# Kernel tuning notes

Hardware: AMD Instinct MI355X
Metric: run time of the kernel (lower is better)

The kernel has to match this reference:

```python
import jax, jax.numpy as jnp
import numpy as np

BN_EPS = 1e-5


def setup_inputs() -> dict:
    key = jax.random.key(0)
    ks = jax.random.split(key, 8)
    N, H, OUT = 32 * 1024, 512, 32
    return {
        "x": jax.random.normal(ks[0], (N, 2), dtype=jnp.float32),
        "batch_size": 32,
        "Wq": jax.random.normal(ks[1], (2, H), dtype=jnp.float32) / np.sqrt(2.0),
        "Wk": jax.random.normal(ks[2], (2, H), dtype=jnp.float32) / np.sqrt(2.0),
        "Wv": jax.random.normal(ks[3], (2, H), dtype=jnp.float32) / np.sqrt(2.0),
        "bn_gamma": jnp.ones((H,), jnp.float32),
        "bn_beta": jnp.zeros((H,), jnp.float32),
        "bn_mean": jnp.zeros((H,), jnp.float32),
        "bn_var": jnp.ones((H,), jnp.float32),
        "prelu_a": jnp.full((1,), 0.25, jnp.float32),
        "W_out": jax.random.normal(ks[4], (H, OUT), dtype=jnp.float32) / np.sqrt(H),
        "b_out": jnp.zeros((OUT,), jnp.float32),
    }


def reference(x, batch_size, Wq, Wk, Wv, bn_gamma, bn_beta, bn_mean, bn_var,
              prelu_a, W_out, b_out):
    H = Wq.shape[1]
    # project tokens [N,2] -> [B,S,H]
    q = (x @ Wq).reshape(batch_size, -1, H)
    k = (x @ Wk).reshape(batch_size, -1, H)
    v = (x @ Wv).reshape(batch_size, -1, H)
    scale = 1.0 / jnp.sqrt(jnp.asarray(H, x.dtype))
    attn = jax.nn.softmax(jnp.einsum("bqh,bkh->bqk", q, k) * scale, axis=-1)
    out = jnp.einsum("bqk,bkh->bqh", attn, v).reshape(-1, H)  # [N,H]
    # BatchNorm1d (eval mode) + PReLU + Linear (dropout = identity in eval)
    out = (out - bn_mean) * (bn_gamma / jnp.sqrt(bn_var + BN_EPS)) + bn_beta
    out = jnp.where(out >= 0, out, prelu_a[0] * out)
    return out @ W_out + b_out
```

## Files before the change

### kernel.cpp

```cpp
#include <hip/hip_runtime.h>
#include <math.h>


#define H_DIM   512
#define OUT_DIM 32
#define S_LEN   1024
#define THREADS 256
#define NW 4

#if __has_builtin(__builtin_amdgcn_exp2f)
#define EXP2(x) __builtin_amdgcn_exp2f(x)
#else
#define EXP2(x) exp2f(x)
#endif

typedef __attribute__((ext_vector_type(8))) short bf16x8;
typedef __attribute__((ext_vector_type(4))) float f32x4;
typedef __attribute__((ext_vector_type(2))) float f32x2;

__device__ __forceinline__ f32x2 pkfma(f32x2 a, f32x2 b, f32x2 c) {
    return __builtin_elementwise_fma(a, b, c);
}
__device__ __forceinline__ unsigned int cvt_pk_bf16(float lo, float hi) {
    unsigned int r;
    asm("v_cvt_pk_bf16_f32 %0, %1, %2" : "=v"(r) : "v"(lo), "v"(hi));
    return r;
}

union frag_cast { unsigned int u[4]; int4 i4; bf16x8 v; };

__global__ __launch_bounds__(THREADS)
void fused_attn_kernel(const float* __restrict__ x,
                       const float* __restrict__ Wq,
                       const float* __restrict__ Wk,
                       const float* __restrict__ Wv,
                       const float* __restrict__ bn_gamma,
                       const float* __restrict__ bn_beta,
                       const float* __restrict__ bn_mean,
                       const float* __restrict__ bn_var,
                       const float* __restrict__ prelu_a,
                       const float* __restrict__ Wout,
                       const float* __restrict__ bout,
                       float* __restrict__ out)
{
    __shared__ __align__(16) float xsx[S_LEN];
    __shared__ __align__(16) float xsy[S_LEN];
    __shared__ float4 a01s[H_DIM / 2];
    __shared__ float2 cps[H_DIM / 2];
    __shared__ unsigned int bfr[32 * 64 * 4];
    __shared__ float redl[NW][64], redw0[NW][64], redw1[NW][64];
    __shared__ float mred[NW][4];

    const int t    = threadIdx.x;
    const int lane = t & 63;
    const int q    = __builtin_amdgcn_readfirstlane(t >> 6);
    const int b    = blockIdx.x >> 4;
    const int tile = blockIdx.x & 15;
    const float scale = 0.044194173824159216f;
    const float L2E   = 1.4426950408889634f;

    const float4* xg = (const float4*)(x + (size_t)b * (S_LEN * 2));
    f32x2* xsx2 = (f32x2*)xsx;
    f32x2* xsy2 = (f32x2*)xsy;
    {
        float4 v0 = xg[t];
        float4 v1 = xg[t + 256];
        f32x2 a = {v0.x, v0.z}; xsx2[t] = a;
        f32x2 c = {v0.y, v0.w}; xsy2[t] = c;
        f32x2 d = {v1.x, v1.z}; xsx2[t + 256] = d;
        f32x2 e = {v1.y, v1.w}; xsy2[t + 256] = e;
    }

    {
        const float2 gm = ((const float2*)bn_gamma)[t];
        const float2 vr = ((const float2*)bn_var)[t];
        const float2 bt = ((const float2*)bn_beta)[t];
        const float2 mn = ((const float2*)bn_mean)[t];
        const float2 wv0 = ((const float2*)Wv)[t];
        const float2 wv1 = ((const float2*)(Wv + H_DIM))[t];
        float g0 = gm.x * rsqrtf(vr.x + 1e-5f);
        float g1 = gm.y * rsqrtf(vr.y + 1e-5f);
        a01s[t] = make_float4(wv0.x * g0, wv0.y * g1, wv1.x * g0, wv1.y * g1);
        cps[t]  = make_float2(bt.x - mn.x * g0, bt.y - mn.y * g1);
    }

    {
        float m00 = 0.f, m01 = 0.f, m10 = 0.f, m11 = 0.f;
        #pragma unroll
        for (int k = 0; k < 2; ++k) {
            int h = t + k * 256;
            float a0 = Wq[h], a1 = Wq[H_DIM + h];
            float b0 = Wk[h], b1 = Wk[H_DIM + h];
            m00 = fmaf(a0, b0, m00); m01 = fmaf(a0, b1, m01);
            m10 = fmaf(a1, b0, m10); m11 = fmaf(a1, b1, m11);
        }
        #pragma unroll
        for (int off = 32; off >= 1; off >>= 1) {
            m00 += __shfl_xor(m00, off); m01 += __shfl_xor(m01, off);
            m10 += __shfl_xor(m10, off); m11 += __shfl_xor(m11, off);
        }
        if (lane == 0) {
            mred[q][0] = m00; mred[q][1] = m01;
            mred[q][2] = m10; mred[q][3] = m11;
        }
    }

    #pragma unroll
    for (int k = 0; k < 32; ++k) {
        int i    = k * 256 + t;
        int c    = i & 15;
        int jj   = (i >> 4) & 3;
        int quad = (i >> 6) & 3;
        int s    = (i >> 8) & 15;
        int nt   = (i >> 12) & 1;
        int h    = s * 32 + quad * 8 + 2 * jj;
        int o    = nt * 16 + c;
        float f0 = Wout[h * 32 + o];
        float f1 = Wout[(h + 1) * 32 + o];
        int F = (nt * 16 + s) * 256 + (quad * 16 + c) * 4 + jj;
        bfr[F] = cvt_pk_bf16(f0, f1);
    }
    __syncthreads();

    float m00 = (mred[0][0] + mred[1][0] + mred[2][0] + mred[3][0]) * scale;
    float m01 = (mred[0][1] + mred[1][1] + mred[2][1] + mred[3][1]) * scale;
    float m10 = (mred[0][2] + mred[1][2] + mred[2][2] + mred[3][2]) * scale;
    float m11 = (mred[0][3] + mred[1][3] + mred[2][3] + mred[3][3]) * scale;

    const float xtx = xsx[tile * 64 + lane];
    const float xty = xsy[tile * 64 + lane];
    const float u0L = fmaf(xtx, m00, xty * m10) * L2E;
    const float u1L = fmaf(xtx, m01, xty * m11) * L2E;
    const f32x2 u0L2 = {u0L, u0L};
    const f32x2 u1L2 = {u1L, u1L};

    f32x2 l2  = {0.f, 0.f};
    f32x2 w02 = {0.f, 0.f};
    f32x2 w12 = {0.f, 0.f};
    const float4* kx4 = (const float4*)(xsx + q * 256);
    const float4* ky4 = (const float4*)(xsy + q * 256);
    #pragma unroll 4
    for (int i = 0; i < 64; ++i) {
        float4 kx = kx4[i];
        float4 ky = ky4[i];
        f32x2 kxa = {kx.x, kx.y};
        f32x2 kxb = {kx.z, kx.w};
        f32x2 kya = {ky.x, ky.y};
        f32x2 kyb = {ky.z, ky.w};
        f32x2 arga = pkfma(u0L2, kxa, u1L2 * kya);
        f32x2 argb = pkfma(u0L2, kxb, u1L2 * kyb);
        f32x2 ea = {EXP2(arga.x), EXP2(arga.y)};
        f32x2 eb = {EXP2(argb.x), EXP2(argb.y)};
        l2  = l2 + ea + eb;
        w02 = pkfma(ea, kxa, w02);
        w02 = pkfma(eb, kxb, w02);
        w12 = pkfma(ea, kya, w12);
        w12 = pkfma(eb, kyb, w12);
    }
    float l  = l2.x + l2.y;
    float w0 = w02.x + w02.y;
    float w1 = w12.x + w12.y;
    redl[q][lane] = l; redw0[q][lane] = w0; redw1[q][lane] = w1;
    __syncthreads();
    l  = redl[0][lane]  + redl[1][lane]  + redl[2][lane]  + redl[3][lane];
    w0 = redw0[0][lane] + redw0[1][lane] + redw0[2][lane] + redw0[3][lane];
    w1 = redw1[0][lane] + redw1[1][lane] + redw1[2][lane] + redw1[3][lane];
    const float inv = 1.0f / l;
    w0 *= inv; w1 *= inv;

    const int src = q * 16 + (lane & 15);
    const float w0t = __shfl(w0, src);
    const float w1t = __shfl(w1, src);
    const f32x2 w0t2 = {w0t, w0t};
    const f32x2 w1t2 = {w1t, w1t};

    const float ap = prelu_a[0];
    const f32x2 ca2 = {0.5f * (1.f + ap), 0.5f * (1.f + ap)};
    const f32x2 cb2 = {0.5f * (1.f - ap), 0.5f * (1.f - ap)};
    const int quad = lane >> 4;
    f32x4 acc0 = {0.f, 0.f, 0.f, 0.f};
    f32x4 acc1 = {0.f, 0.f, 0.f, 0.f};
    const int4* bsrc = (const int4*)bfr;

    for (int s = 0; s < 16; ++s) {
        frag_cast bf0, bf1;
        bf0.i4 = bsrc[s * 64 + lane];
        bf1.i4 = bsrc[(16 + s) * 64 + lane];
        const int hb2 = s * 16 + quad * 4;
        frag_cast af;
        #pragma unroll
        for (int jj = 0; jj < 4; ++jj) {
            float4 a = a01s[hb2 + jj];
            float2 c = cps[hb2 + jj];
            f32x2 a0 = {a.x, a.y};
            f32x2 a1 = {a.z, a.w};
            f32x2 cc = {c.x, c.y};
            f32x2 z  = pkfma(w0t2, a0, pkfma(w1t2, a1, cc));
            f32x2 az = __builtin_elementwise_abs(z);
            f32x2 p  = pkfma(ca2, z, cb2 * az);
            af.u[jj] = cvt_pk_bf16(p.x, p.y);
        }
        acc0 = __builtin_amdgcn_mfma_f32_16x16x32_bf16(af.v, bf0.v, acc0, 0, 0, 0);
        acc1 = __builtin_amdgcn_mfma_f32_16x16x32_bf16(af.v, bf1.v, acc1, 0, 0, 0);
    }

    const size_t base = (size_t)(b * S_LEN + tile * 64) * OUT_DIM;
    const int o0 = lane & 15;
    const float bo0 = bout[o0], bo1 = bout[16 + o0];
    #pragma unroll
    for (int r = 0; r < 4; ++r) {
        const int tt = q * 16 + quad * 4 + r;
        out[base + tt * 32 + o0]      = acc0[r] + bo0;
        out[base + tt * 32 + 16 + o0] = acc1[r] + bo1;
    }
}

extern "C" void kernel_launch(void* const* d_in, const int* in_sizes, int n_in,
                              void* d_out, int out_size, void* d_ws, size_t ws_size,
                              hipStream_t stream) {
    const float* x    = (const float*)d_in[0];
    const float* Wq   = (const float*)d_in[2];
    const float* Wk   = (const float*)d_in[3];
    const float* Wv   = (const float*)d_in[4];
    const float* gam  = (const float*)d_in[5];
    const float* bet  = (const float*)d_in[6];
    const float* mean = (const float*)d_in[7];
    const float* var  = (const float*)d_in[8];
    const float* pa   = (const float*)d_in[9];
    const float* Wout = (const float*)d_in[10];
    const float* bo   = (const float*)d_in[11];
    float* out = (float*)d_out;

    const int N = in_sizes[0] / 2;
    const int blocks = N / 64;
    hipLaunchKernelGGL(fused_attn_kernel, dim3(blocks), dim3(THREADS), 0, stream,
                       x, Wq, Wk, Wv, gam, bet, mean, var, pa, Wout, bo, out);
}
```

Before: 87.93 us.

## Split keys across lane groups within each wave and reduce with shuffles

Work is remapped so each wave owns 16 queries, and the four 16-lane groups inside the wave each scan a quarter of the keys. The partial softmax sums are then combined with xor-shuffles instead of an LDS reduction followed by a block-wide barrier. This also removes the later cross-lane shuffle that redistributed per-query weights. The x/y shared arrays are padded by four floats per 256-key quarter so the four groups' float4 reads land in different banks. The cost is that key reads are no longer a single broadcast address per wave but four distinct addresses.

```diff
diff --git a/kernel.cpp b/kernel.cpp
--- a/kernel.cpp
+++ b/kernel.cpp
@@ -5,6 +5,8 @@
 #define H_DIM   512
 #define OUT_DIM 32
 #define S_LEN   1024
+#define QSTRIDE 260
+#define XS_LEN  1040
 #define THREADS 256
 #define NW 4
 
@@ -43,12 +45,11 @@
                        const float* __restrict__ bout,
                        float* __restrict__ out)
 {
-    __shared__ __align__(16) float xsx[S_LEN];
-    __shared__ __align__(16) float xsy[S_LEN];
+    __shared__ __align__(16) float xsx[XS_LEN];
+    __shared__ __align__(16) float xsy[XS_LEN];
     __shared__ float4 a01s[H_DIM / 2];
     __shared__ float2 cps[H_DIM / 2];
     __shared__ unsigned int bfr[32 * 64 * 4];
-    __shared__ float redl[NW][64], redw0[NW][64], redw1[NW][64];
     __shared__ float mred[NW][4];
 
     const int t    = threadIdx.x;
@@ -65,10 +66,12 @@
     {
         float4 v0 = xg[t];
         float4 v1 = xg[t + 256];
-        f32x2 a = {v0.x, v0.z}; xsx2[t] = a;
-        f32x2 c = {v0.y, v0.w}; xsy2[t] = c;
-        f32x2 d = {v1.x, v1.z}; xsx2[t + 256] = d;
-        f32x2 e = {v1.y, v1.w}; xsy2[t + 256] = e;
+        const int i0 = t + (t >> 7) * 2;
+        const int i1 = (t + 256) + ((t >> 7) + 2) * 2;
+        f32x2 a = {v0.x, v0.z}; xsx2[i0] = a;
+        f32x2 cy = {v0.y, v0.w}; xsy2[i0] = cy;
+        f32x2 d = {v1.x, v1.z}; xsx2[i1] = d;
+        f32x2 e = {v1.y, v1.w}; xsy2[i1] = e;
     }
 
     {
@@ -127,8 +130,12 @@
     float m10 = (mred[0][2] + mred[1][2] + mred[2][2] + mred[3][2]) * scale;
     float m11 = (mred[0][3] + mred[1][3] + mred[2][3] + mred[3][3]) * scale;
 
-    const float xtx = xsx[tile * 64 + lane];
-    const float xty = xsy[tile * 64 + lane];
+    const int m  = lane & 15;
+    const int g  = lane >> 4;
+    const int jt = tile * 64 + q * 16 + m;
+    const int jo = jt + ((jt >> 8) << 2);
+    const float xtx = xsx[jo];
+    const float xty = xsy[jo];
     const float u0L = fmaf(xtx, m00, xty * m10) * L2E;
     const float u1L = fmaf(xtx, m01, xty * m11) * L2E;
     const f32x2 u0L2 = {u0L, u0L};
@@ -137,8 +144,8 @@
     f32x2 l2  = {0.f, 0.f};
     f32x2 w02 = {0.f, 0.f};
     f32x2 w12 = {0.f, 0.f};
-    const float4* kx4 = (const float4*)(xsx + q * 256);
-    const float4* ky4 = (const float4*)(xsy + q * 256);
+    const float4* kx4 = (const float4*)(xsx + g * QSTRIDE);
+    const float4* ky4 = (const float4*)(xsy + g * QSTRIDE);
     #pragma unroll 4
     for (int i = 0; i < 64; ++i) {
         float4 kx = kx4[i];
@@ -160,17 +167,12 @@
     float l  = l2.x + l2.y;
     float w0 = w02.x + w02.y;
     float w1 = w12.x + w12.y;
-    redl[q][lane] = l; redw0[q][lane] = w0; redw1[q][lane] = w1;
-    __syncthreads();
-    l  = redl[0][lane]  + redl[1][lane]  + redl[2][lane]  + redl[3][lane];
-    w0 = redw0[0][lane] + redw0[1][lane] + redw0[2][lane] + redw0[3][lane];
-    w1 = redw1[0][lane] + redw1[1][lane] + redw1[2][lane] + redw1[3][lane];
+    l  += __shfl_xor(l, 16);  l  += __shfl_xor(l, 32);
+    w0 += __shfl_xor(w0, 16); w0 += __shfl_xor(w0, 32);
+    w1 += __shfl_xor(w1, 16); w1 += __shfl_xor(w1, 32);
     const float inv = 1.0f / l;
-    w0 *= inv; w1 *= inv;
-
-    const int src = q * 16 + (lane & 15);
-    const float w0t = __shfl(w0, src);
-    const float w1t = __shfl(w1, src);
+    const float w0t = w0 * inv;
+    const float w1t = w1 * inv;
     const f32x2 w0t2 = {w0t, w0t};
     const f32x2 w1t2 = {w1t, w1t};
 
@@ -191,10 +193,10 @@
         #pragma unroll
         for (int jj = 0; jj < 4; ++jj) {
             float4 a = a01s[hb2 + jj];
-            float2 c = cps[hb2 + jj];
+            float2 cc2 = cps[hb2 + jj];
             f32x2 a0 = {a.x, a.y};
             f32x2 a1 = {a.z, a.w};
-            f32x2 cc = {c.x, c.y};
+            f32x2 cc = {cc2.x, cc2.y};
             f32x2 z  = pkfma(w0t2, a0, pkfma(w1t2, a1, cc));
             f32x2 az = __builtin_elementwise_abs(z);
             f32x2 p  = pkfma(ca2, z, cb2 * az);
```

Result: no change. 88.31 us (+0.4%).
